# Kernel tuning notes

Hardware: AMD Instinct MI355X
Metric: run time of the kernel (lower is better)

Reference implementation:

```python
import jax, jax.numpy as jnp
import numpy as np

PATCH = 64
STRIDE = PATCH // 2
SEQ = 65536
NPATCH = (SEQ - PATCH) // STRIDE + 1  # 2047
B = 256
EPS = 1e-5


def setup_inputs() -> dict:
    key = jax.random.key(0)
    ks = jax.random.split(key, 10)
    s = lambda k, shp: jax.random.normal(k, shp, jnp.float32) * 0.05
    return dict(
        x=jax.random.normal(ks[0], (B, 1, SEQ), jnp.float32),
        conv1_w=s(ks[1], (NPATCH, NPATCH - 1)),
        conv1_b=s(ks[2], (NPATCH,)),
        w1=s(ks[3], (32, 3, 5)), b1=s(ks[4], (32,)),
        g1=jnp.ones((32,), jnp.float32), be1=jnp.zeros((32,), jnp.float32),
        w2=s(ks[5], (64, 32, 3)), b2=s(ks[6], (64,)),
        g2=jnp.ones((64,), jnp.float32), be2=jnp.zeros((64,), jnp.float32),
        w3=s(ks[7], (128, 64, 3)), b3=s(ks[8], (128,)),
        g3=jnp.ones((128,), jnp.float32), be3=jnp.zeros((128,), jnp.float32),
    )


def _conv1d(x, w, b, pad):
    # x: [B, Cin, L], w: [Cout, Cin, K]
    y = jax.lax.conv_general_dilated(x, w, (1,), [(pad, pad)],
                                     dimension_numbers=('NCH', 'OIH', 'NCH'))
    return y + b[None, :, None]


def _bn(x, g, be):
    # training-mode BatchNorm1d: biased var over (batch, length)
    m = jnp.mean(x, axis=(0, 2), keepdims=True)
    v = jnp.var(x, axis=(0, 2), keepdims=True)
    return (x - m) * jax.lax.rsqrt(v + EPS) * g[None, :, None] + be[None, :, None]


def _maxpool2(x):
    # MaxPool1d(kernel=2, stride=2), floor division of length
    L = x.shape[-1] // 2
    return x[..., : 2 * L].reshape(x.shape[0], x.shape[1], L, 2).max(-1)


def reference(x, conv1_w, conv1_b, w1, b1, g1, be1, w2, b2, g2, be2, w3, b3, g3, be3):
    starts = jnp.arange(NPATCH) * STRIDE
    idx = starts[:, None] + jnp.arange(PATCH)[None, :]         # [NW, W]
    xp = x[:, :, idx]                                          # [B,1,NW,W]
    mean = xp.mean(-1)                                         # [B,1,NW]
    std = jnp.std(xp, axis=-1, ddof=1)                         # torch.std is unbiased
    stats = jnp.concatenate([mean, std], axis=1)               # [B,2,NW]
    dx = jnp.diff(xp, axis=2)                                  # diff across window index: [B,1,NW-1,W]
    dmax = dx.max(-1)                                          # [B,1,NW-1]
    dmax = jnp.transpose(dmax, (0, 2, 1))                      # [B,NW-1,1]
    # conv1: 1x1 Conv1d over length-1 axis == matmul over channel dim
    d2 = jnp.einsum('oi,bil->bol', conv1_w, dmax) + conv1_b[None, :, None]  # [B,NW,1]
    d2 = jnp.transpose(d2, (0, 2, 1))                          # [B,1,NW]
    x3 = jnp.concatenate([stats, d2], axis=1)                  # [B,3,NW]
    h = _maxpool2(jax.nn.relu(_bn(_conv1d(x3, w1, b1, 2), g1, be1)))
    h = _maxpool2(jax.nn.relu(_bn(_conv1d(h, w2, b2, 1), g2, be2)))
    h = jax.nn.relu(_bn(_conv1d(h, w3, b3, 1), g3, be3))
    return h.mean(-1)                                          # AdaptiveAvgPool1d(1)+Flatten -> [B,128]
```

## Files before the change

kernel.cpp:

```cpp
#include <hip/hip_runtime.h>
#include <math.h>

#define NB 256
#define SEQ 65536
#define NP 2047
#define NPM 2046
#define NPP 2048
#define KPAD 2048
#define LEN1 2047
#define LEN2 1023
#define LEN3 511
#define C1 32
#define C2 64
#define C3 128
#define NPART 2048
#define NPART2 (NB*4)
#define LPAD 514

#define OFF_X3   0
#define SZ_X3    (NB*3*NPP)
#define OFF_DMAX (OFF_X3 + SZ_X3)
#define SZ_DMAX  (NB*NPM)
#define OFF_Y1   (OFF_DMAX + SZ_DMAX)
#define SZ_Y1    (NB*C1*LEN1)
#define OFF_Y2   (OFF_Y1 + SZ_Y1)
#define SZ_Y2    (NB*C2*LEN2)
#define OFF_S1   (OFF_Y2 + SZ_Y2)
#define OFF_S2   (OFF_S1 + 2*C1)
#define OFF_S3   (OFF_S2 + 2*C2)
#define OFF_W2C  (OFF_S3 + 2*C3)
#define OFF_W3B  (OFF_W2C + C1*C2*3)
#define OFF_PS   (OFF_W3B + C2*C3*3)
#define OFF_PQ   (OFF_PS + C3*NPART)
#define OFF_WB   OFF_Y2
#define OFF_H1R  OFF_Y2
#define OFF_H2T  OFF_Y2
#define OFF_PM   (OFF_Y1 + 4300000)
#define OFF_W2B  OFF_W2C

typedef __attribute__((ext_vector_type(8))) short short8;
typedef __attribute__((ext_vector_type(4))) float f32x4;

__device__ inline short f2bf(float f){
  union { float f; unsigned u; } x; x.f = f;
  unsigned r = x.u + 0x7FFF + ((x.u >> 16) & 1);
  return (short)(r >> 16);
}

#define RED4L(v) v += __shfl_xor(v,1,64); v += __shfl_xor(v,2,64); \
                 v += __shfl_xor(v,4,64); v += __shfl_xor(v,8,64);

#define TILES(X) X(0,0) X(0,1) X(0,2) X(0,3) X(1,0) X(1,1) X(1,2) X(1,3) \
                 X(2,0) X(2,1) X(2,2) X(2,3) X(3,0) X(3,1) X(3,2) X(3,3)
#define DECLBIAS(P,ct) f32x4 bi##ct = *(const f32x4*)((P) + cbase + ct*16 + kq*4);
#define DECLACC(lt,ct) f32x4 acc##lt##ct = bi##ct;

__global__ __launch_bounds__(256) void k_patch(const float* __restrict__ x, const float* __restrict__ c1b,
                                               float* __restrict__ ws){
  float* x3    = ws + OFF_X3;
  short* dmaxB = (short*)(ws + OFF_DMAX);
  int b = blockIdx.y;
  int chunk = blockIdx.x;
  const float* xr = x + (size_t)b*SEQ + chunk*2048;
  __shared__ float Ss[65], Qs[65], Dm[65];
  int w = threadIdx.x >> 6;
  int l = threadIdx.x & 63;
  #pragma unroll
  for (int i=0;i<2;i++){
    int seg = w*2 + i;
    int off = seg*256;
    float4 A = *(const float4*)(xr + off + l*4);
    float4 Bh = make_float4(0.f,0.f,0.f,0.f);
    if (l >= 56){
      int g = chunk*2048 + off + 256 + (l-56)*4;
      if (g + 3 < SEQ) Bh = *(const float4*)(xr + off + 256 + (l-56)*4);
    }
    int src = (l+8) & 63;
    float p0 = __shfl(A.x, src, 64), p1 = __shfl(A.y, src, 64),
          p2 = __shfl(A.z, src, 64), p3 = __shfl(A.w, src, 64);
    if (l >= 56){ p0=Bh.x; p1=Bh.y; p2=Bh.z; p3=Bh.w; }
    float s = (A.x+A.y)+(A.z+A.w);
    float q = fmaf(A.x,A.x, fmaf(A.y,A.y, fmaf(A.z,A.z, A.w*A.w)));
    float d = fmaxf(fmaxf(p0-A.x, p1-A.y), fmaxf(p2-A.z, p3-A.w));
    #pragma unroll
    for (int o=1;o<8;o<<=1){
      s += __shfl_xor(s,o,64);
      q += __shfl_xor(q,o,64);
      d  = fmaxf(d, __shfl_xor(d,o,64));
    }
    if ((l&7)==0){ int m = seg*8 + (l>>3); Ss[m]=s; Qs[m]=q; Dm[m]=d; }
  }
  if (w==0){
    float s=0.f,q=0.f,d=-1e30f;
    if (l < 8){
      int g = chunk*2048 + 2048 + l*4;
      if (g+3 < SEQ){
        float4 A = *(const float4*)(xr + 2048 + l*4);
        float4 P = make_float4(0.f,0.f,0.f,0.f);
        if (g+35 < SEQ) P = *(const float4*)(xr + 2048 + 32 + l*4);
        s = (A.x+A.y)+(A.z+A.w);
        q = fmaf(A.x,A.x, fmaf(A.y,A.y, fmaf(A.z,A.z, A.w*A.w)));
        d = fmaxf(fmaxf(P.x-A.x, P.y-A.y), fmaxf(P.z-A.z, P.w-A.w));
      }
    }
    #pragma unroll
    for (int o=1;o<8;o<<=1){
      s += __shfl_xor(s,o,64);
      q += __shfl_xor(q,o,64);
      d  = fmaxf(d, __shfl_xor(d,o,64));
    }
    if (l==0){ Ss[64]=s; Qs[64]=q; Dm[64]=d; }
  }
  __syncthreads();
  if (threadIdx.x < 64){
    int j = threadIdx.x;
    int p = chunk*64 + j;
    if (p < NP){
      float S = Ss[j]+Ss[j+1];
      float Q = Qs[j]+Qs[j+1];
      float mean = S*(1.0f/64.0f);
      float var  = (Q - S*mean)*(1.0f/63.0f);
      x3[(size_t)(b*3+0)*NPP + p] = mean;
      x3[(size_t)(b*3+1)*NPP + p] = sqrtf(fmaxf(var,0.0f));
      x3[(size_t)(b*3+2)*NPP + p] = c1b[p];
    }
    dmaxB[(size_t)b*KPAD + p] = (p < NPM) ? f2bf(fmaxf(Dm[j], Dm[j+1])) : (short)0;
  }
}

__global__ __launch_bounds__(256) void k_prep(const float* __restrict__ W, const float* __restrict__ w2,
                                              const float* __restrict__ w3, float* __restrict__ ws){
  int bid = blockIdx.x;
  if (bid < 8*NP){
    short* Wb = (short*)(ws + OFF_WB);
    int o = bid >> 3;
    int k = (bid & 7)*256 + threadIdx.x;
    Wb[(size_t)o*KPAD + k] = (k < NPM) ? f2bf(W[(size_t)o*NPM + k]) : (short)0;
  } else {
    short* w2b = (short*)(ws + OFF_W2B);
    short* w3b = (short*)(ws + OFF_W3B);
    int t = (bid - 8*NP)*256 + threadIdx.x;
    if (t < 3*C2*C1){
      int tap = t / (C2*C1);
      int r = t - tap*(C2*C1);
      int c = r >> 5, i = r & 31;
      w2b[t] = f2bf(w2[(c*C1 + i)*3 + tap]);
    }
    if (t < 3*C3*C2){
      int tap = t / (C3*C2);
      int r = t - tap*(C3*C2);
      int c = r / C2, i = r - c*C2;
      w3b[(tap*C3 + c)*C2 + i] = f2bf(w3[(c*C2+i)*3 + tap]);
    }
  }
}

__global__ __launch_bounds__(256) void k_gemm(float* __restrict__ ws){
  const short* Ab = (const short*)(ws + OFF_DMAX);
  const short* Bb = (const short*)(ws + OFF_WB);
  float* x3 = ws + OFF_X3;
  int wid  = __builtin_amdgcn_readfirstlane(threadIdx.x >> 6);
  int lane = threadIdx.x & 63;
  int ln = lane & 15, kq = lane >> 4;
  int n0  = blockIdx.x*32;
  int m16 = (blockIdx.y*4 + wid)*16;
  int ks  = blockIdx.z*512;
  f32x4 acc0 = {0.f,0.f,0.f,0.f}, acc1 = {0.f,0.f,0.f,0.f};
  int o0 = n0 + ln, o1 = n0 + 16 + ln;
  const short* ap  = Ab + (size_t)(m16 + ln)*KPAD + ks + kq*8;
  const short* bp0 = Bb + (size_t)min(o0, NP-1)*KPAD + ks + kq*8;
  const short* bp1 = Bb + (size_t)min(o1, NP-1)*KPAD + ks + kq*8;
  #pragma unroll 4
  for (int s=0; s<16; s++){
    short8 av = *(const short8*)(ap  + s*32);
    short8 b0 = *(const short8*)(bp0 + s*32);
    short8 b1 = *(const short8*)(bp1 + s*32);
    acc0 = __builtin_amdgcn_mfma_f32_16x16x32_bf16(av, b0, acc0, 0, 0, 0);
    acc1 = __builtin_amdgcn_mfma_f32_16x16x32_bf16(av, b1, acc1, 0, 0, 0);
  }
  #pragma unroll
  for (int r=0;r<4;r++){
    int b = m16 + kq*4 + r;
    float* xp = x3 + ((size_t)(b*3) + 2)*NPP;
    if (o0 < NP) atomicAdd(xp + o0, acc0[r]);
    if (o1 < NP) atomicAdd(xp + o1, acc1[r]);
  }
}

__global__ __launch_bounds__(256) void k_conv1f(const float* __restrict__ w1, const float* __restrict__ b1, float* __restrict__ ws){
  const float* x3 = ws + OFF_X3;
  float* h1r = ws + OFF_H1R;
  float* ps = ws + OFF_PS;
  float* pq = ws + OFF_PQ;
  int b = blockIdx.y;
  int blk = blockIdx.x;
  int w = threadIdx.x >> 6;
  int lane = threadIdx.x & 63;
  int h = lane >> 5, c = lane & 31;
  int p0 = blk*256 + w*64 + h*32;
  float wv[3][5];
  #pragma unroll
  for (int i=0;i<3;i++){
    #pragma unroll
    for (int j=0;j<5;j++) wv[i][j] = w1[(c*3+i)*5+j];
  }
  float bc = b1[c];
  const float* xb = x3 + (size_t)b*3*NPP;
  float s = 0.f, q = 0.f;
  #pragma unroll
  for (int k0=0;k0<32;k0+=8){
    int base = p0 + k0 - 4;
    float xw[3][16];
    #pragma unroll
    for (int i=0;i<3;i++){
      const float* xr = xb + (size_t)i*NPP;
      if (base >= 0 && base + 16 <= LEN1){
        #pragma unroll
        for (int t=0;t<4;t++) *(f32x4*)&xw[i][4*t] = *(const f32x4*)(xr + base + 4*t);
      } else {
        #pragma unroll
        for (int t=0;t<16;t++){ int g = base + t; xw[i][t] = (g >= 0 && g < LEN1) ? xr[g] : 0.f; }
      }
    }
    float acc[8];
    #pragma unroll
    for (int k=0;k<8;k++){
      float a = bc;
      #pragma unroll
      for (int i=0;i<3;i++){
        #pragma unroll
        for (int j=0;j<5;j++) a = fmaf(wv[i][j], xw[i][k+j+2], a);
      }
      acc[k] = a;
      if (p0 + k0 + k < LEN1){ s += a; q = fmaf(a, a, q); }
    }
    #pragma unroll
    for (int t=0;t<4;t++){
      int m = ((p0 + k0) >> 1) + t;
      if (m < LEN2) h1r[((size_t)b*LEN2 + m)*C1 + c] = fmaxf(acc[2*t], acc[2*t+1]);
    }
  }
  s += __shfl_xor(s, 32, 64);
  q += __shfl_xor(q, 32, 64);
  __shared__ float es[4][C1], eq[4][C1];
  if (h == 0){ es[w][c] = s; eq[w][c] = q; }
  __syncthreads();
  if (threadIdx.x < C1){
    int cc = threadIdx.x;
    float S = es[0][cc]+es[1][cc]+es[2][cc]+es[3][cc];
    float Q = eq[0][cc]+eq[1][cc]+eq[2][cc]+eq[3][cc];
    ps[(size_t)cc*NPART + b*8 + blk] = S;
    pq[(size_t)cc*NPART + b*8 + blk] = Q;
  }
}

__global__ __launch_bounds__(256) void k_fin(const float* __restrict__ ps, const float* __restrict__ pq,
                                             const float* __restrict__ g, const float* __restrict__ be,
                                             float* __restrict__ stats, int C, int npart, double invN,
                                             float* __restrict__ outz){
  if (outz) outz[(size_t)threadIdx.x * C3 + blockIdx.x] = 0.f;
  int c = blockIdx.x;
  double s=0.0, q=0.0;
  for (int j=threadIdx.x; j<npart; j+=256){ s += (double)ps[c*npart+j]; q += (double)pq[c*npart+j]; }
  #pragma unroll
  for (int off=32; off; off>>=1){ s += __shfl_xor(s,off,64); q += __shfl_xor(q,off,64); }
  __shared__ double rs[4], rq[4];
  int wid = threadIdx.x>>6, lane=threadIdx.x&63;
  if (lane==0){ rs[wid]=s; rq[wid]=q; }
  __syncthreads();
  if (threadIdx.x==0){
    double S = rs[0]+rs[1]+rs[2]+rs[3];
    double Q = rq[0]+rq[1]+rq[2]+rq[3];
    double mean = S*invN;
    double var  = Q*invN - mean*mean;
    double a = (double)g[c] / sqrt(var + 1e-5);
    stats[c]   = (float)a;
    stats[C+c] = (float)((double)be[c] - mean*a);
  }
}

__global__ __launch_bounds__(256) void k_conv2m(const float* __restrict__ b2, float* __restrict__ ws){
  const float* h1r = ws + OFF_H1R;
  const float* st1 = ws + OFF_S1;
  const short* w2b = (const short*)(ws + OFF_W2B);
  float* pmaxT = ws + OFF_PM;
  float* ps = ws + OFF_PS;
  float* pq = ws + OFF_PQ;
  int b   = blockIdx.y;
  int blk = blockIdx.x;
  int w   = __builtin_amdgcn_readfirstlane(threadIdx.x >> 6);
  int lane = threadIdx.x & 63;
  int ln = lane & 15, kq = lane >> 4;
  int l0 = blk*256 + w*64;
  int cbase = 0;
  DECLBIAS(b2,0) DECLBIAS(b2,1) DECLBIAS(b2,2) DECLBIAS(b2,3)
  TILES(DECLACC)
  f32x4 a1lo = *(const f32x4*)(st1 + kq*8),      a1hi = *(const f32x4*)(st1 + kq*8 + 4);
  f32x4 b1lo = *(const f32x4*)(st1 + C1 + kq*8), b1hi = *(const f32x4*)(st1 + C1 + kq*8 + 4);
  const short* wA = w2b + (size_t)ln*C1 + kq*8;
#define LDW(T,ct) short8 aw##T##ct = *(const short8*)(wA + (size_t)(T*C2 + ct*16)*C1);
  LDW(0,0) LDW(0,1) LDW(0,2) LDW(0,3)
  LDW(1,0) LDW(1,1) LDW(1,2) LDW(1,3)
  LDW(2,0) LDW(2,1) LDW(2,2) LDW(2,3)
#undef LDW
  const float* hR = h1r + (size_t)b*LEN2*C1 + kq*8;
#define MMT0(lt,ct) acc##lt##ct = __builtin_amdgcn_mfma_f32_16x16x32_bf16(aw0##ct, bv##lt, acc##lt##ct, 0, 0, 0);
#define MMT1(lt,ct) acc##lt##ct = __builtin_amdgcn_mfma_f32_16x16x32_bf16(aw1##ct, bv##lt, acc##lt##ct, 0, 0, 0);
#define MMT2(lt,ct) acc##lt##ct = __builtin_amdgcn_mfma_f32_16x16x32_bf16(aw2##ct, bv##lt, acc##lt##ct, 0, 0, 0);
#define LDB(lt,T) short8 bv##lt; { \
    int pos_ = l0 + ln + lt*16 + T - 1; \
    union { short8 s8; short s[8]; } fr_; \
    if (pos_ >= 0 && pos_ < LEN2){ \
      const float* pa_ = hR + (size_t)pos_*C1; \
      f32x4 xlo_ = *(const f32x4*)pa_, xhi_ = *(const f32x4*)(pa_ + 4); \
      fr_.s[0] = f2bf(fmaxf(fmaf(a1lo[0], xlo_[0], b1lo[0]), 0.f)); \
      fr_.s[1] = f2bf(fmaxf(fmaf(a1lo[1], xlo_[1], b1lo[1]), 0.f)); \
      fr_.s[2] = f2bf(fmaxf(fmaf(a1lo[2], xlo_[2], b1lo[2]), 0.f)); \
      fr_.s[3] = f2bf(fmaxf(fmaf(a1lo[3], xlo_[3], b1lo[3]), 0.f)); \
      fr_.s[4] = f2bf(fmaxf(fmaf(a1hi[0], xhi_[0], b1hi[0]), 0.f)); \
      fr_.s[5] = f2bf(fmaxf(fmaf(a1hi[1], xhi_[1], b1hi[1]), 0.f)); \
      fr_.s[6] = f2bf(fmaxf(fmaf(a1hi[2], xhi_[2], b1hi[2]), 0.f)); \
      fr_.s[7] = f2bf(fmaxf(fmaf(a1hi[3], xhi_[3], b1hi[3]), 0.f)); \
    } else { fr_.s8 = (short8)0; } \
    bv##lt = fr_.s8; }
#define CSTEP(T) { \
    LDB(0,T) LDB(1,T) LDB(2,T) LDB(3,T) \
    TILES(MMT##T) }
  CSTEP(0) CSTEP(1) CSTEP(2)
#undef CSTEP
#undef LDB
#define PST(lt,ct) { \
    float p0_ = fmaxf(acc##lt##ct[0], __shfl_xor(acc##lt##ct[0],1,64)); \
    float p1_ = fmaxf(acc##lt##ct[1], __shfl_xor(acc##lt##ct[1],1,64)); \
    float p2_ = fmaxf(acc##lt##ct[2], __shfl_xor(acc##lt##ct[2],1,64)); \
    float p3_ = fmaxf(acc##lt##ct[3], __shfl_xor(acc##lt##ct[3],1,64)); \
    int l_ = l0 + lt*16 + ln; \
    if (!(ln & 1) && (l_ >> 1) < LEN3){ \
      f32x4 pv_ = {p0_, p1_, p2_, p3_}; \
      *(f32x4*)(pmaxT + ((size_t)b*LEN3 + (l_>>1))*C2 + ct*16 + kq*4) = pv_; } }
  TILES(PST)
#undef PST
  __shared__ float es[4][C2], eq[4][C2];
  #pragma unroll
  for (int ct=0;ct<4;ct++){
    float s0=0.f,s1=0.f,s2=0.f,s3=0.f,q0=0.f,q1=0.f,q2=0.f,q3=0.f;
#define ACCST(lt,CT) if (CT == ct){ int l_ = l0 + lt*16 + ln; if (l_ < LEN2){ \
      s0 += acc##lt##CT[0]; q0 = fmaf(acc##lt##CT[0], acc##lt##CT[0], q0); \
      s1 += acc##lt##CT[1]; q1 = fmaf(acc##lt##CT[1], acc##lt##CT[1], q1); \
      s2 += acc##lt##CT[2]; q2 = fmaf(acc##lt##CT[2], acc##lt##CT[2], q2); \
      s3 += acc##lt##CT[3]; q3 = fmaf(acc##lt##CT[3], acc##lt##CT[3], q3); } }
    TILES(ACCST)
#undef ACCST
    RED4L(s0) RED4L(s1) RED4L(s2) RED4L(s3)
    RED4L(q0) RED4L(q1) RED4L(q2) RED4L(q3)
    if (ln == 0){
      int c0 = ct*16 + kq*4;
      es[w][c0+0]=s0; es[w][c0+1]=s1; es[w][c0+2]=s2; es[w][c0+3]=s3;
      eq[w][c0+0]=q0; eq[w][c0+1]=q1; eq[w][c0+2]=q2; eq[w][c0+3]=q3;
    }
  }
  __syncthreads();
  if (threadIdx.x < C2){
    int c = threadIdx.x;
    float S = es[0][c]+es[1][c]+es[2][c]+es[3][c];
    float Q = eq[0][c]+eq[1][c]+eq[2][c]+eq[3][c];
    ps[(size_t)c*NPART2 + b*4 + blk] = S;
    pq[(size_t)c*NPART2 + b*4 + blk] = Q;
  }
}

__global__ __launch_bounds__(256) void k_p2bf(float* __restrict__ ws){
  const float* pm = ws + OFF_PM;
  const float* st = ws + OFF_S2;
  short* h2t = (short*)(ws + OFF_H2T);
  int b = blockIdx.y;
  int idx = blockIdx.x*256 + threadIdx.x;
  if (idx < LEN3*C2){
    int m = idx >> 6, c = idx & 63;
    float v = fmaxf(fmaf(st[c], pm[((size_t)b*LEN3 + m)*C2 + c], st[C2+c]), 0.f);
    h2t[((size_t)b*LPAD + m + 1)*C2 + c] = f2bf(v);
  } else {
    int zr = idx - LEN3*C2;
    if (zr < 3*C2){
      int rsel = zr >> 6, c = zr & 63;
      int row = (rsel == 0) ? 0 : (511 + rsel);
      h2t[((size_t)b*LPAD + row)*C2 + c] = 0;
    }
  }
}

__global__ __launch_bounds__(256) void k_conv3s(const float* __restrict__ b3, float* __restrict__ ws){
  const short* h2t = (const short*)(ws + OFF_H2T);
  const short* w3b = (const short*)(ws + OFF_W3B);
  float* ps = ws + OFF_PS;
  float* pq = ws + OFF_PQ;
  int b   = blockIdx.y;
  int blk = blockIdx.x;
  int wid = __builtin_amdgcn_readfirstlane(threadIdx.x >> 6);
  int lane = threadIdx.x & 63;
  int ln = lane & 15, kq = lane >> 4;
  int lh = wid & 1, ch = wid >> 1;
  int l0 = blk*128 + lh*64;
  int cbase = ch*64;
  DECLBIAS(b3,0) DECLBIAS(b3,1) DECLBIAS(b3,2) DECLBIAS(b3,3)
  TILES(DECLACC)
  const short* hB = h2t + ((size_t)b*LPAD + l0 + ln)*C2 + kq*8;
  const short* wA = w3b + (size_t)(cbase + ln)*C2 + kq*8;
  #pragma unroll
  for (int t=0;t<3;t++){
    #pragma unroll
    for (int s=0;s<2;s++){
#define LDB(lt) short8 bv##lt = *(const short8*)(hB + (size_t)(lt*16 + t)*C2 + s*32);
      LDB(0) LDB(1) LDB(2) LDB(3)
#define LDA(ct) short8 av##ct = *(const short8*)(wA + (size_t)(t*C3 + ct*16)*C2 + s*32);
      LDA(0) LDA(1) LDA(2) LDA(3)
#define MM(lt,ct) acc##lt##ct = __builtin_amdgcn_mfma_f32_16x16x32_bf16(av##ct, bv##lt, acc##lt##ct, 0, 0, 0);
      TILES(MM)
#undef LDB
#undef LDA
    }
  }
  int pidx = b*8 + blk*2 + lh;
  #pragma unroll
  for (int ct=0;ct<4;ct++){
    float s0=0.f,s1=0.f,s2=0.f,s3=0.f,q0=0.f,q1=0.f,q2=0.f,q3=0.f;
#define ACCST(lt,CT) if (CT == ct){ int l_ = l0 + lt*16 + ln; if (l_ < LEN3){ \
      s0 += acc##lt##CT[0]; q0 = fmaf(acc##lt##CT[0], acc##lt##CT[0], q0); \
      s1 += acc##lt##CT[1]; q1 = fmaf(acc##lt##CT[1], acc##lt##CT[1], q1); \
      s2 += acc##lt##CT[2]; q2 = fmaf(acc##lt##CT[2], acc##lt##CT[2], q2); \
      s3 += acc##lt##CT[3]; q3 = fmaf(acc##lt##CT[3], acc##lt##CT[3], q3); } }
    TILES(ACCST)
#undef ACCST
    RED4L(s0) RED4L(s1) RED4L(s2) RED4L(s3)
    RED4L(q0) RED4L(q1) RED4L(q2) RED4L(q3)
    if (ln == 0){
      int c0 = cbase + ct*16 + kq*4;
      ps[(size_t)(c0+0)*NPART + pidx] = s0;  pq[(size_t)(c0+0)*NPART + pidx] = q0;
      ps[(size_t)(c0+1)*NPART + pidx] = s1;  pq[(size_t)(c0+1)*NPART + pidx] = q1;
      ps[(size_t)(c0+2)*NPART + pidx] = s2;  pq[(size_t)(c0+2)*NPART + pidx] = q2;
      ps[(size_t)(c0+3)*NPART + pidx] = s3;  pq[(size_t)(c0+3)*NPART + pidx] = q3;
    }
  }
}

__global__ __launch_bounds__(256) void k_out3(float* __restrict__ out, const float* __restrict__ b3,
                                              const float* __restrict__ ws){
  const short* h2t = (const short*)(ws + OFF_H2T);
  const short* w3b = (const short*)(ws + OFF_W3B);
  const float* st  = ws + OFF_S3;
  int b   = blockIdx.y;
  int blk = blockIdx.x;
  int wid = __builtin_amdgcn_readfirstlane(threadIdx.x >> 6);
  int lane = threadIdx.x & 63;
  int ln = lane & 15, kq = lane >> 4;
  int lh = wid & 1, ch = wid >> 1;
  int l0 = blk*128 + lh*64;
  int cbase = ch*64;
  DECLBIAS(b3,0) DECLBIAS(b3,1) DECLBIAS(b3,2) DECLBIAS(b3,3)
  TILES(DECLACC)
  const short* hB = h2t + ((size_t)b*LPAD + l0 + ln)*C2 + kq*8;
  const short* wA = w3b + (size_t)(cbase + ln)*C2 + kq*8;
  #pragma unroll
  for (int t=0;t<3;t++){
    #pragma unroll
    for (int s=0;s<2;s++){
#define LDB(lt) short8 bv##lt = *(const short8*)(hB + (size_t)(lt*16 + t)*C2 + s*32);
      LDB(0) LDB(1) LDB(2) LDB(3)
#define LDA(ct) short8 av##ct = *(const short8*)(wA + (size_t)(t*C3 + ct*16)*C2 + s*32);
      LDA(0) LDA(1) LDA(2) LDA(3)
      TILES(MM)
#undef LDB
#undef LDA
    }
  }
  const float inv = 1.0f/511.0f;
  #pragma unroll
  for (int ct=0;ct<4;ct++){
    int c0 = cbase + ct*16 + kq*4;
    float a0 = st[c0+0], a1 = st[c0+1], a2 = st[c0+2], a3 = st[c0+3];
    float h0 = st[C3+c0+0], h1_ = st[C3+c0+1], h2_ = st[C3+c0+2], h3 = st[C3+c0+3];
    float s0=0.f,s1=0.f,s2=0.f,s3=0.f;
#define OSUM(lt,CT) if (CT == ct){ int l_ = l0 + lt*16 + ln; if (l_ < LEN3){ \
      s0 += fmaxf(fmaf(a0, acc##lt##CT[0], h0 ), 0.f); \
      s1 += fmaxf(fmaf(a1, acc##lt##CT[1], h1_), 0.f); \
      s2 += fmaxf(fmaf(a2, acc##lt##CT[2], h2_), 0.f); \
      s3 += fmaxf(fmaf(a3, acc##lt##CT[3], h3 ), 0.f); } }
    TILES(OSUM)
#undef OSUM
    RED4L(s0) RED4L(s1) RED4L(s2) RED4L(s3)
    if (ln == 0){
      atomicAdd(out + (size_t)b*C3 + c0+0, s0*inv);
      atomicAdd(out + (size_t)b*C3 + c0+1, s1*inv);
      atomicAdd(out + (size_t)b*C3 + c0+2, s2*inv);
      atomicAdd(out + (size_t)b*C3 + c0+3, s3*inv);
    }
  }
}

extern "C" void kernel_launch(void* const* d_in, const int* in_sizes, int n_in,
                              void* d_out, int out_size, void* d_ws, size_t ws_size,
                              hipStream_t stream) {
  const float* x   = (const float*)d_in[0];
  const float* c1w = (const float*)d_in[1];
  const float* c1b = (const float*)d_in[2];
  const float* w1  = (const float*)d_in[3];
  const float* b1  = (const float*)d_in[4];
  const float* g1  = (const float*)d_in[5];
  const float* be1 = (const float*)d_in[6];
  const float* w2  = (const float*)d_in[7];
  const float* b2  = (const float*)d_in[8];
  const float* g2  = (const float*)d_in[9];
  const float* be2 = (const float*)d_in[10];
  const float* w3  = (const float*)d_in[11];
  const float* b3  = (const float*)d_in[12];
  const float* g3  = (const float*)d_in[13];
  const float* be3 = (const float*)d_in[14];
  float* ws  = (float*)d_ws;
  float* out = (float*)d_out;

  hipLaunchKernelGGL(k_patch,  dim3(32,NB), dim3(256), 0, stream, x, c1b, ws);
  hipLaunchKernelGGL(k_prep,   dim3(8*NP + 96), dim3(256), 0, stream, c1w, w2, w3, ws);
  hipLaunchKernelGGL(k_gemm,   dim3(64,4,4), dim3(256), 0, stream, ws);
  hipLaunchKernelGGL(k_conv1f, dim3(8,NB), dim3(256), 0, stream, w1, b1, ws);
  hipLaunchKernelGGL(k_fin,    dim3(C1), dim3(256), 0, stream, ws+OFF_PS, ws+OFF_PQ, g1, be1, ws+OFF_S1, C1, NPART, 1.0/((double)NB*LEN1), (float*)nullptr);
  hipLaunchKernelGGL(k_conv2m, dim3(4,NB), dim3(256), 0, stream, b2, ws);
  hipLaunchKernelGGL(k_fin,    dim3(C2), dim3(256), 0, stream, ws+OFF_PS, ws+OFF_PQ, g2, be2, ws+OFF_S2, C2, NPART2, 1.0/((double)NB*LEN2), (float*)nullptr);
  hipLaunchKernelGGL(k_p2bf,   dim3((LEN3*C2+3*C2+255)/256, NB), dim3(256), 0, stream, ws);
  hipLaunchKernelGGL(k_conv3s, dim3(4,NB), dim3(256), 0, stream, b3, ws);
  hipLaunchKernelGGL(k_fin,    dim3(C3), dim3(256), 0, stream, ws+OFF_PS, ws+OFF_PQ, g3, be3, ws+OFF_S3, C3, NPART, 1.0/((double)NB*LEN3), out);
  hipLaunchKernelGGL(k_out3,   dim3(4,NB), dim3(256), 0, stream, out, b3, ws);
}
```

Measured before the change: 302.5 us.

## Stage normalized conv2 input in LDS and block h2 layout by channel groups

k_conv2m now loads the 258-row window of h1 once per block, applies the BN affine, ReLU and bf16 conversion cooperatively, and stores it in padded shared memory. The MFMA B operands are then read from LDS, which removes the redundant global loads and repeated normalization across the three taps and overlapping waves. Separately, the h2t buffer is rearranged into channel-group-major [b][c/8][pos][8] blocks so conv3 B-fragment loads read contiguous 16-byte rows along position. This adds a __syncthreads and about 20 KB of LDS per block, which may reduce occupancy.

```diff
diff --git a/kernel.cpp b/kernel.cpp
--- a/kernel.cpp
+++ b/kernel.cpp
@@ -16,6 +16,7 @@
 #define NPART 2048
 #define NPART2 (NB*4)
 #define LPAD 514
+#define SROW 40
 
 #define OFF_X3   0
 #define SZ_X3    (NB*3*NPP)
@@ -39,6 +40,7 @@
 #define OFF_W2B  OFF_W2C
 
 typedef __attribute__((ext_vector_type(8))) short short8;
+typedef __attribute__((ext_vector_type(4))) short short4v;
 typedef __attribute__((ext_vector_type(4))) float f32x4;
 
 __device__ inline short f2bf(float f){
@@ -288,53 +290,49 @@
   float* pq = ws + OFF_PQ;
   int b   = blockIdx.y;
   int blk = blockIdx.x;
+  int l0  = blk*256;
+  __shared__ __align__(16) short sh[258*SROW];
+  for (int u = threadIdx.x; u < 258*8; u += 256){
+    int row = u >> 3, g = u & 7;
+    int pos = l0 - 1 + row;
+    short4v r4 = (short4v)0;
+    if (pos >= 0 && pos < LEN2){
+      f32x4 xv = *(const f32x4*)(h1r + ((size_t)b*LEN2 + pos)*C1 + g*4);
+      f32x4 av = *(const f32x4*)(st1 + g*4);
+      f32x4 bb = *(const f32x4*)(st1 + C1 + g*4);
+      #pragma unroll
+      for (int j=0;j<4;j++) r4[j] = f2bf(fmaxf(fmaf(av[j], xv[j], bb[j]), 0.f));
+    }
+    *(short4v*)(sh + row*SROW + g*4) = r4;
+  }
+  __syncthreads();
   int w   = __builtin_amdgcn_readfirstlane(threadIdx.x >> 6);
   int lane = threadIdx.x & 63;
   int ln = lane & 15, kq = lane >> 4;
-  int l0 = blk*256 + w*64;
+  int lw = l0 + w*64;
   int cbase = 0;
   DECLBIAS(b2,0) DECLBIAS(b2,1) DECLBIAS(b2,2) DECLBIAS(b2,3)
   TILES(DECLACC)
-  f32x4 a1lo = *(const f32x4*)(st1 + kq*8),      a1hi = *(const f32x4*)(st1 + kq*8 + 4);
-  f32x4 b1lo = *(const f32x4*)(st1 + C1 + kq*8), b1hi = *(const f32x4*)(st1 + C1 + kq*8 + 4);
   const short* wA = w2b + (size_t)ln*C1 + kq*8;
 #define LDW(T,ct) short8 aw##T##ct = *(const short8*)(wA + (size_t)(T*C2 + ct*16)*C1);
   LDW(0,0) LDW(0,1) LDW(0,2) LDW(0,3)
   LDW(1,0) LDW(1,1) LDW(1,2) LDW(1,3)
   LDW(2,0) LDW(2,1) LDW(2,2) LDW(2,3)
 #undef LDW
-  const float* hR = h1r + (size_t)b*LEN2*C1 + kq*8;
 #define MMT0(lt,ct) acc##lt##ct = __builtin_amdgcn_mfma_f32_16x16x32_bf16(aw0##ct, bv##lt, acc##lt##ct, 0, 0, 0);
 #define MMT1(lt,ct) acc##lt##ct = __builtin_amdgcn_mfma_f32_16x16x32_bf16(aw1##ct, bv##lt, acc##lt##ct, 0, 0, 0);
 #define MMT2(lt,ct) acc##lt##ct = __builtin_amdgcn_mfma_f32_16x16x32_bf16(aw2##ct, bv##lt, acc##lt##ct, 0, 0, 0);
-#define LDB(lt,T) short8 bv##lt; { \
-    int pos_ = l0 + ln + lt*16 + T - 1; \
-    union { short8 s8; short s[8]; } fr_; \
-    if (pos_ >= 0 && pos_ < LEN2){ \
-      const float* pa_ = hR + (size_t)pos_*C1; \
-      f32x4 xlo_ = *(const f32x4*)pa_, xhi_ = *(const f32x4*)(pa_ + 4); \
-      fr_.s[0] = f2bf(fmaxf(fmaf(a1lo[0], xlo_[0], b1lo[0]), 0.f)); \
-      fr_.s[1] = f2bf(fmaxf(fmaf(a1lo[1], xlo_[1], b1lo[1]), 0.f)); \
-      fr_.s[2] = f2bf(fmaxf(fmaf(a1lo[2], xlo_[2], b1lo[2]), 0.f)); \
-      fr_.s[3] = f2bf(fmaxf(fmaf(a1lo[3], xlo_[3], b1lo[3]), 0.f)); \
-      fr_.s[4] = f2bf(fmaxf(fmaf(a1hi[0], xhi_[0], b1hi[0]), 0.f)); \
-      fr_.s[5] = f2bf(fmaxf(fmaf(a1hi[1], xhi_[1], b1hi[1]), 0.f)); \
-      fr_.s[6] = f2bf(fmaxf(fmaf(a1hi[2], xhi_[2], b1hi[2]), 0.f)); \
-      fr_.s[7] = f2bf(fmaxf(fmaf(a1hi[3], xhi_[3], b1hi[3]), 0.f)); \
-    } else { fr_.s8 = (short8)0; } \
-    bv##lt = fr_.s8; }
-#define CSTEP(T) { \
-    LDB(0,T) LDB(1,T) LDB(2,T) LDB(3,T) \
-    TILES(MMT##T) }
+#define LDB2(lt,T) short8 bv##lt = *(const short8*)(sh + (size_t)(w*64 + lt*16 + T + ln)*SROW + kq*8);
+#define CSTEP(T) { LDB2(0,T) LDB2(1,T) LDB2(2,T) LDB2(3,T) TILES(MMT##T) }
   CSTEP(0) CSTEP(1) CSTEP(2)
 #undef CSTEP
-#undef LDB
+#undef LDB2
 #define PST(lt,ct) { \
     float p0_ = fmaxf(acc##lt##ct[0], __shfl_xor(acc##lt##ct[0],1,64)); \
     float p1_ = fmaxf(acc##lt##ct[1], __shfl_xor(acc##lt##ct[1],1,64)); \
     float p2_ = fmaxf(acc##lt##ct[2], __shfl_xor(acc##lt##ct[2],1,64)); \
     float p3_ = fmaxf(acc##lt##ct[3], __shfl_xor(acc##lt##ct[3],1,64)); \
-    int l_ = l0 + lt*16 + ln; \
+    int l_ = lw + lt*16 + ln; \
     if (!(ln & 1) && (l_ >> 1) < LEN3){ \
       f32x4 pv_ = {p0_, p1_, p2_, p3_}; \
       *(f32x4*)(pmaxT + ((size_t)b*LEN3 + (l_>>1))*C2 + ct*16 + kq*4) = pv_; } }
@@ -344,7 +342,7 @@
   #pragma unroll
   for (int ct=0;ct<4;ct++){
     float s0=0.f,s1=0.f,s2=0.f,s3=0.f,q0=0.f,q1=0.f,q2=0.f,q3=0.f;
-#define ACCST(lt,CT) if (CT == ct){ int l_ = l0 + lt*16 + ln; if (l_ < LEN2){ \
+#define ACCST(lt,CT) if (CT == ct){ int l_ = lw + lt*16 + ln; if (l_ < LEN2){ \
       s0 += acc##lt##CT[0]; q0 = fmaf(acc##lt##CT[0], acc##lt##CT[0], q0); \
       s1 += acc##lt##CT[1]; q1 = fmaf(acc##lt##CT[1], acc##lt##CT[1], q1); \
       s2 += acc##lt##CT[2]; q2 = fmaf(acc##lt##CT[2], acc##lt##CT[2], q2); \
@@ -378,13 +376,13 @@
   if (idx < LEN3*C2){
     int m = idx >> 6, c = idx & 63;
     float v = fmaxf(fmaf(st[c], pm[((size_t)b*LEN3 + m)*C2 + c], st[C2+c]), 0.f);
-    h2t[((size_t)b*LPAD + m + 1)*C2 + c] = f2bf(v);
+    h2t[(((size_t)b*8 + (c>>3))*LPAD + m + 1)*8 + (c&7)] = f2bf(v);
   } else {
     int zr = idx - LEN3*C2;
     if (zr < 3*C2){
       int rsel = zr >> 6, c = zr & 63;
       int row = (rsel == 0) ? 0 : (511 + rsel);
-      h2t[((size_t)b*LPAD + row)*C2 + c] = 0;
+      h2t[(((size_t)b*8 + (c>>3))*LPAD + row)*8 + (c&7)] = 0;
     }
   }
 }
@@ -404,13 +402,13 @@
   int cbase = ch*64;
   DECLBIAS(b3,0) DECLBIAS(b3,1) DECLBIAS(b3,2) DECLBIAS(b3,3)
   TILES(DECLACC)
-  const short* hB = h2t + ((size_t)b*LPAD + l0 + ln)*C2 + kq*8;
+  const short* hB = h2t + (((size_t)b*8 + kq)*LPAD + l0 + ln)*8;
   const short* wA = w3b + (size_t)(cbase + ln)*C2 + kq*8;
   #pragma unroll
   for (int t=0;t<3;t++){
     #pragma unroll
     for (int s=0;s<2;s++){
-#define LDB(lt) short8 bv##lt = *(const short8*)(hB + (size_t)(lt*16 + t)*C2 + s*32);
+#define LDB(lt) short8 bv##lt = *(const short8*)(hB + ((size_t)s*4*LPAD + lt*16 + t)*8);
       LDB(0) LDB(1) LDB(2) LDB(3)
 #define LDA(ct) short8 av##ct = *(const short8*)(wA + (size_t)(t*C3 + ct*16)*C2 + s*32);
       LDA(0) LDA(1) LDA(2) LDA(3)
@@ -458,13 +456,13 @@
   int cbase = ch*64;
   DECLBIAS(b3,0) DECLBIAS(b3,1) DECLBIAS(b3,2) DECLBIAS(b3,3)
   TILES(DECLACC)
-  const short* hB = h2t + ((size_t)b*LPAD + l0 + ln)*C2 + kq*8;
+  const short* hB = h2t + (((size_t)b*8 + kq)*LPAD + l0 + ln)*8;
   const short* wA = w3b + (size_t)(cbase + ln)*C2 + kq*8;
   #pragma unroll
   for (int t=0;t<3;t++){
     #pragma unroll
     for (int s=0;s<2;s++){
-#define LDB(lt) short8 bv##lt = *(const short8*)(hB + (size_t)(lt*16 + t)*C2 + s*32);
+#define LDB(lt) short8 bv##lt = *(const short8*)(hB + ((size_t)s*4*LPAD + lt*16 + t)*8);
       LDB(0) LDB(1) LDB(2) LDB(3)
 #define LDA(ct) short8 av##ct = *(const short8*)(wA + (size_t)(t*C3 + ct*16)*C2 + s*32);
       LDA(0) LDA(1) LDA(2) LDA(3)
```

Result: faster. 289.2 us (-4.4%).
